# Kernel optimization log

Measured on AMD Instinct MI355X. Metric: run time of the kernel, lower is better.

Reference implementation:

```python
import jax, jax.numpy as jnp
import numpy as np

B, S, D, E = 4, 2048, 512, 32

def setup_inputs() -> dict:
    key = jax.random.key(0)
    k1, k2, k3 = jax.random.split(key, 3)
    x = jax.random.normal(k1, (B, S, D), dtype=jnp.float32)
    # glorot-ish scaling for weights
    gate_w = jax.random.normal(k2, (D, E), dtype=jnp.float32) * (1.0 / np.sqrt(D))
    gate_b = jnp.zeros((E,), dtype=jnp.float32)
    expert_w = jax.random.normal(k3, (E, D, D), dtype=jnp.float32) * (1.0 / np.sqrt(D))
    return {"x": x, "gate_w": gate_w, "gate_b": gate_b, "expert_w": expert_w}

def reference(x, gate_w, gate_b, expert_w):
    # gate_scores: [B,S,E] (context=None -> route on x itself)
    gate = jax.nn.softmax(jnp.einsum('bsd,de->bse', x, gate_w) + gate_b, axis=-1)
    # Dense soft-MoE: sum_e gate[b,s,e] * (x[b,s,:] @ expert_w[e])
    # Single einsum avoids materializing the [B,S,E,D] intermediate.
    out = jnp.einsum('bse,bsd,edf->bsf', gate, x, expert_w)
    return out
```

## Files before the change

kernel.cpp:

```cpp
#include <hip/hip_runtime.h>

#define TOK 8192
#define DIM 512
#define NE  32
#define KTOT (NE * DIM)

#define BM 128
#define BN 128
#define BK 64

typedef float f32x4 __attribute__((ext_vector_type(4)));
typedef short s16x8 __attribute__((ext_vector_type(8)));

typedef const void __attribute__((address_space(1)))* gp1_t;
typedef void __attribute__((address_space(3)))* lp3_t;

__device__ __forceinline__ void gl_lds16(const void* g, void* l) {
    __builtin_amdgcn_global_load_lds((gp1_t)g, (lp3_t)l, 16, 0, 0);
}

__device__ __forceinline__ ushort f2bf(float f) {
    unsigned u = __builtin_bit_cast(unsigned, f);
    unsigned r = (u + 0x7fffu + ((u >> 16) & 1u)) >> 16;
    return (ushort)r;
}

__global__ __launch_bounds__(256) void k_prep(const float* __restrict__ w,
                                              ushort* __restrict__ wt,
                                              const float* __restrict__ x,
                                              const float* __restrict__ gw,
                                              const float* __restrict__ gb,
                                              float* __restrict__ G,
                                              ushort* __restrict__ xb) {
    __shared__ __align__(16) char smem[64 * 65 * 4];
    const int bx = blockIdx.x;
    const int tid = threadIdx.x;
    if (bx < 2048) {
        float (*tile)[65] = (float(*)[65])smem;
        const int e = bx >> 6;
        const int f0 = ((bx >> 3) & 7) * 64;
        const int d0 = (bx & 7) * 64;
        const int tx = tid & 63, ty = tid >> 6;
        const float* we = w + (size_t)e * DIM * DIM;
#pragma unroll
        for (int i = ty; i < 64; i += 4)
            tile[i][tx] = we[(size_t)(d0 + i) * DIM + f0 + tx];
        __syncthreads();
#pragma unroll
        for (int i = ty; i < 64; i += 4)
            wt[(size_t)(f0 + i) * KTOT + e * DIM + d0 + tx] = f2bf(tile[tx][i]);
    } else {
        float* xs = (float*)smem;
        const int t0 = (bx - 2048) * 8;
        const float* xBase = x + (size_t)t0 * DIM;
#pragma unroll
        for (int k = 0; k < 4; ++k) {
            int i4 = (k * 256 + tid) * 4;
            float4 v = *(const float4*)(xBase + i4);
            xs[i4 + 0] = v.x; xs[i4 + 1] = v.y; xs[i4 + 2] = v.z; xs[i4 + 3] = v.w;
            ushort4 o;
            o.x = f2bf(v.x); o.y = f2bf(v.y); o.z = f2bf(v.z); o.w = f2bf(v.w);
            *(ushort4*)(xb + (size_t)t0 * DIM + i4) = o;
        }
        __syncthreads();
        const int tok = tid >> 5;
        const int e = tid & 31;
        float l = gb[e];
        const float* xr = xs + tok * DIM;
#pragma unroll 8
        for (int d = 0; d < DIM; ++d)
            l += xr[d] * gw[d * NE + e];
        float mx = l;
#pragma unroll
        for (int m = 16; m >= 1; m >>= 1) mx = fmaxf(mx, __shfl_xor(mx, m));
        float ex = expf(l - mx);
        float s = ex;
#pragma unroll
        for (int m = 16; m >= 1; m >>= 1) s += __shfl_xor(s, m);
        G[(size_t)(t0 + tok) * NE + e] = ex / s;
    }
}

__global__ __launch_bounds__(512, 2) void k_moe_gemm(const ushort* __restrict__ xb,
                                                     const ushort* __restrict__ wt,
                                                     const float* __restrict__ G,
                                                     float* __restrict__ out0,
                                                     float* __restrict__ out1) {
    __shared__ __align__(16) ushort As[2][BM * BK];
    __shared__ __align__(16) ushort Bs[2][BN * BK];
    __shared__ float Gs[16][BM];

    const int tid = threadIdx.x;
    const int m0 = blockIdx.y * BM;
    const int n0 = blockIdx.x * BN;
    const int e0 = blockIdx.z * 16;
    float* __restrict__ dst = blockIdx.z ? out1 : out0;

    for (int i = tid; i < 16 * BM; i += 512) {
        int e = i >> 7, r = i & 127;
        Gs[e][r] = G[(size_t)(m0 + r) * NE + e0 + e];
    }

    const int lane = tid & 63;
    const int wave = tid >> 6;
    const int wm = (wave & 3) * 32;
    const int wn = (wave >> 2) * 64;
    const int l15 = lane & 15;
    const int q = lane >> 4;
    const int keyR = l15 & 7;

    const int swz0 = ((q) ^ keyR) * 16;
    const int swz1 = ((4 + q) ^ keyR) * 16;
    const int rowA0 = (wm + l15) * 128;
    const int rowA1 = (wm + 16 + l15) * 128;
    const int rowB0 = (wn + l15) * 128;
    const int rowB1 = (wn + 16 + l15) * 128;
    const int rowB2 = (wn + 32 + l15) * 128;
    const int rowB3 = (wn + 48 + l15) * 128;

    const int srow = tid >> 3;
    const int chunk = tid & 7;
    const int scol = ((chunk ^ (srow & 7)) * 8);
    const ushort* aBase = xb + (size_t)(m0 + srow) * DIM + scol;
    const ushort* bBase = wt + (size_t)(n0 + srow) * KTOT + (size_t)e0 * DIM + scol;
    const int ldsOff = tid * 16;

    const f32x4 zv = {0.f, 0.f, 0.f, 0.f};
    f32x4 acc[2][4];
#pragma unroll
    for (int i = 0; i < 2; ++i)
#pragma unroll
        for (int j = 0; j < 4; ++j) acc[i][j] = zv;

    gl_lds16(aBase, (char*)As[0] + ldsOff);
    gl_lds16(aBase + (size_t)64 * DIM, (char*)As[0] + 8192 + ldsOff);
    gl_lds16(bBase, (char*)Bs[0] + ldsOff);
    gl_lds16(bBase + (size_t)64 * KTOT, (char*)Bs[0] + 8192 + ldsOff);
    __syncthreads();

#pragma unroll 1
    for (int kt = 0; kt < 8; ++kt) {
        const char* Ab = (const char*)As[kt & 1];
#pragma unroll 1
        for (int ee = 0; ee < 16; ++ee) {
            const int gn = kt * 16 + ee + 1;
            if (gn < 128) {
                const ushort* bN = bBase + (size_t)(gn & 15) * DIM + (gn >> 4) * BK;
                char* bL = (char*)Bs[gn & 1] + ldsOff;
                gl_lds16(bN, bL);
                gl_lds16(bN + (size_t)64 * KTOT, bL + 8192);
                if (ee == 15) {
                    const ushort* aN = aBase + (kt + 1) * BK;
                    char* aL = (char*)As[(kt + 1) & 1] + ldsOff;
                    gl_lds16(aN, aL);
                    gl_lds16(aN + (size_t)64 * DIM, aL + 8192);
                }
            }

            const char* Bb = (const char*)Bs[ee & 1];
            f32x4 pacc[2][4];
#pragma unroll
            for (int ks = 0; ks < 2; ++ks) {
                const int swz = ks ? swz1 : swz0;
                s16x8 a0 = *(const s16x8*)(Ab + rowA0 + swz);
                s16x8 a1 = *(const s16x8*)(Ab + rowA1 + swz);
                s16x8 b0 = *(const s16x8*)(Bb + rowB0 + swz);
                s16x8 b1 = *(const s16x8*)(Bb + rowB1 + swz);
                s16x8 b2 = *(const s16x8*)(Bb + rowB2 + swz);
                s16x8 b3 = *(const s16x8*)(Bb + rowB3 + swz);
                if (ks == 0) {
                    pacc[0][0] = __builtin_amdgcn_mfma_f32_16x16x32_bf16(a0, b0, zv, 0, 0, 0);
                    pacc[0][1] = __builtin_amdgcn_mfma_f32_16x16x32_bf16(a0, b1, zv, 0, 0, 0);
                    pacc[0][2] = __builtin_amdgcn_mfma_f32_16x16x32_bf16(a0, b2, zv, 0, 0, 0);
                    pacc[0][3] = __builtin_amdgcn_mfma_f32_16x16x32_bf16(a0, b3, zv, 0, 0, 0);
                    pacc[1][0] = __builtin_amdgcn_mfma_f32_16x16x32_bf16(a1, b0, zv, 0, 0, 0);
                    pacc[1][1] = __builtin_amdgcn_mfma_f32_16x16x32_bf16(a1, b1, zv, 0, 0, 0);
                    pacc[1][2] = __builtin_amdgcn_mfma_f32_16x16x32_bf16(a1, b2, zv, 0, 0, 0);
                    pacc[1][3] = __builtin_amdgcn_mfma_f32_16x16x32_bf16(a1, b3, zv, 0, 0, 0);
                } else {
                    pacc[0][0] = __builtin_amdgcn_mfma_f32_16x16x32_bf16(a0, b0, pacc[0][0], 0, 0, 0);
                    pacc[0][1] = __builtin_amdgcn_mfma_f32_16x16x32_bf16(a0, b1, pacc[0][1], 0, 0, 0);
                    pacc[0][2] = __builtin_amdgcn_mfma_f32_16x16x32_bf16(a0, b2, pacc[0][2], 0, 0, 0);
                    pacc[0][3] = __builtin_amdgcn_mfma_f32_16x16x32_bf16(a0, b3, pacc[0][3], 0, 0, 0);
                    pacc[1][0] = __builtin_amdgcn_mfma_f32_16x16x32_bf16(a1, b0, pacc[1][0], 0, 0, 0);
                    pacc[1][1] = __builtin_amdgcn_mfma_f32_16x16x32_bf16(a1, b1, pacc[1][1], 0, 0, 0);
                    pacc[1][2] = __builtin_amdgcn_mfma_f32_16x16x32_bf16(a1, b2, pacc[1][2], 0, 0, 0);
                    pacc[1][3] = __builtin_amdgcn_mfma_f32_16x16x32_bf16(a1, b3, pacc[1][3], 0, 0, 0);
                }
            }

#pragma unroll
            for (int i = 0; i < 2; ++i) {
                const f32x4 gt = *(const f32x4*)&Gs[ee][wm + i * 16 + q * 4];
#pragma unroll
                for (int j = 0; j < 4; ++j) {
                    acc[i][j][0] += gt[0] * pacc[i][j][0];
                    acc[i][j][1] += gt[1] * pacc[i][j][1];
                    acc[i][j][2] += gt[2] * pacc[i][j][2];
                    acc[i][j][3] += gt[3] * pacc[i][j][3];
                }
            }
            __syncthreads();
        }
    }

#pragma unroll
    for (int i = 0; i < 2; ++i) {
        const int tl = m0 + wm + i * 16 + q * 4;
#pragma unroll
        for (int j = 0; j < 4; ++j) {
            const int f = n0 + wn + j * 16 + l15;
            float* p = dst + (size_t)tl * DIM + f;
            p[0 * DIM] = acc[i][j][0];
            p[1 * DIM] = acc[i][j][1];
            p[2 * DIM] = acc[i][j][2];
            p[3 * DIM] = acc[i][j][3];
        }
    }
}

__global__ __launch_bounds__(256) void k_reduce(float* __restrict__ out,
                                                const float* __restrict__ P) {
    int i = (blockIdx.x * 256 + threadIdx.x) * 4;
    float4 a = *(const float4*)(out + i);
    float4 b = *(const float4*)(P + i);
    a.x += b.x; a.y += b.y; a.z += b.z; a.w += b.w;
    *(float4*)(out + i) = a;
}

extern "C" void kernel_launch(void* const* d_in, const int* in_sizes, int n_in,
                              void* d_out, int out_size, void* d_ws, size_t ws_size,
                              hipStream_t stream) {
    const float* x  = (const float*)d_in[0];
    const float* gw = (const float*)d_in[1];
    const float* gb = (const float*)d_in[2];
    const float* w  = (const float*)d_in[3];
    float* out = (float*)d_out;

    char* ws = (char*)d_ws;
    ushort* xb = (ushort*)ws;
    ushort* wt = (ushort*)(ws + (8u << 20));
    float*  G  = (float*)(ws + (24u << 20));
    float*  P  = (float*)(ws + (25u << 20));

    k_prep<<<dim3(2048 + TOK / 8), dim3(256), 0, stream>>>(w, wt, x, gw, gb, G, xb);
    k_moe_gemm<<<dim3(DIM / BN, TOK / BM, 2), dim3(512), 0, stream>>>(xb, wt, G, out, P);
    k_reduce<<<dim3(TOK * DIM / 1024), dim3(256), 0, stream>>>(out, P);
}
```

Baseline: 257.9 us.

## Switch MoE GEMM to 32x32x16 MFMA with 4 waves and register-cached A

Restructures the GEMM block from 8 waves of 32x64 tiles using 16x16x32 MFMA to 4 waves of 64x64 tiles using 32x32x16 MFMA. The A fragments are loaded from LDS once per k-tile and kept in registers across all 16 experts, and each wave reuses its operands over a larger output tile. The aim is to cut LDS reads and issue overhead per flop. In exchange, register pressure rises (4 f32x16 accumulators plus cached A) and there are fewer waves per block to hide latency.

```diff
diff --git a/kernel.cpp b/kernel.cpp
--- a/kernel.cpp
+++ b/kernel.cpp
@@ -9,14 +9,22 @@
 #define BN 128
 #define BK 64
 
-typedef float f32x4 __attribute__((ext_vector_type(4)));
-typedef short s16x8 __attribute__((ext_vector_type(8)));
+typedef float f32x4  __attribute__((ext_vector_type(4)));
+typedef float f32x16 __attribute__((ext_vector_type(16)));
+typedef short s16x8  __attribute__((ext_vector_type(8)));
 
 typedef const void __attribute__((address_space(1)))* gp1_t;
 typedef void __attribute__((address_space(3)))* lp3_t;
 
 __device__ __forceinline__ void gl_lds16(const void* g, void* l) {
     __builtin_amdgcn_global_load_lds((gp1_t)g, (lp3_t)l, 16, 0, 0);
+}
+
+__device__ __forceinline__ void stage4(const ushort* g, size_t gstride, char* l) {
+    gl_lds16(g,               l);
+    gl_lds16(g + gstride,     l + 4096);
+    gl_lds16(g + 2 * gstride, l + 8192);
+    gl_lds16(g + 3 * gstride, l + 12288);
 }
 
 __device__ __forceinline__ ushort f2bf(float f) {
@@ -81,7 +89,7 @@
     }
 }
 
-__global__ __launch_bounds__(512, 2) void k_moe_gemm(const ushort* __restrict__ xb,
+__global__ __launch_bounds__(256, 2) void k_moe_gemm(const ushort* __restrict__ xb,
                                                      const ushort* __restrict__ wt,
                                                      const float* __restrict__ G,
                                                      float* __restrict__ out0,
@@ -96,108 +104,93 @@
     const int e0 = blockIdx.z * 16;
     float* __restrict__ dst = blockIdx.z ? out1 : out0;
 
-    for (int i = tid; i < 16 * BM; i += 512) {
+    for (int i = tid; i < 16 * BM; i += 256) {
         int e = i >> 7, r = i & 127;
         Gs[e][r] = G[(size_t)(m0 + r) * NE + e0 + e];
     }
 
     const int lane = tid & 63;
     const int wave = tid >> 6;
-    const int wm = (wave & 3) * 32;
-    const int wn = (wave >> 2) * 64;
-    const int l15 = lane & 15;
-    const int q = lane >> 4;
-    const int keyR = l15 & 7;
-
-    const int swz0 = ((q) ^ keyR) * 16;
-    const int swz1 = ((4 + q) ^ keyR) * 16;
-    const int rowA0 = (wm + l15) * 128;
-    const int rowA1 = (wm + 16 + l15) * 128;
-    const int rowB0 = (wn + l15) * 128;
-    const int rowB1 = (wn + 16 + l15) * 128;
-    const int rowB2 = (wn + 32 + l15) * 128;
-    const int rowB3 = (wn + 48 + l15) * 128;
+    const int wm = (wave & 1) * 64;
+    const int wn = (wave >> 1) * 64;
+    const int l31 = lane & 31;
+    const int hi = lane >> 5;
+    const int key = l31 & 7;
+
+    int chunkOff[4], rowOffA[2], rowOffB[2];
+#pragma unroll
+    for (int s = 0; s < 4; ++s) chunkOff[s] = ((2 * s + hi) ^ key) * 16;
+#pragma unroll
+    for (int i = 0; i < 2; ++i) {
+        rowOffA[i] = (wm + i * 32 + l31) * 128;
+        rowOffB[i] = (wn + i * 32 + l31) * 128;
+    }
 
     const int srow = tid >> 3;
-    const int chunk = tid & 7;
-    const int scol = ((chunk ^ (srow & 7)) * 8);
+    const int scol = ((tid & 7) ^ (srow & 7)) * 8;
     const ushort* aBase = xb + (size_t)(m0 + srow) * DIM + scol;
     const ushort* bBase = wt + (size_t)(n0 + srow) * KTOT + (size_t)e0 * DIM + scol;
     const int ldsOff = tid * 16;
 
-    const f32x4 zv = {0.f, 0.f, 0.f, 0.f};
-    f32x4 acc[2][4];
+    f32x16 zv16;
+#pragma unroll
+    for (int j = 0; j < 16; ++j) zv16[j] = 0.f;
+    f32x16 acc[2][2];
 #pragma unroll
     for (int i = 0; i < 2; ++i)
 #pragma unroll
-        for (int j = 0; j < 4; ++j) acc[i][j] = zv;
-
-    gl_lds16(aBase, (char*)As[0] + ldsOff);
-    gl_lds16(aBase + (size_t)64 * DIM, (char*)As[0] + 8192 + ldsOff);
-    gl_lds16(bBase, (char*)Bs[0] + ldsOff);
-    gl_lds16(bBase + (size_t)64 * KTOT, (char*)Bs[0] + 8192 + ldsOff);
+        for (int j = 0; j < 2; ++j) acc[i][j] = zv16;
+
+    stage4(aBase, (size_t)32 * DIM,  (char*)As[0] + ldsOff);
+    stage4(bBase, (size_t)32 * KTOT, (char*)Bs[0] + ldsOff);
     __syncthreads();
 
 #pragma unroll 1
     for (int kt = 0; kt < 8; ++kt) {
         const char* Ab = (const char*)As[kt & 1];
+        s16x8 areg[2][4];
+#pragma unroll
+        for (int mi = 0; mi < 2; ++mi)
+#pragma unroll
+            for (int s = 0; s < 4; ++s)
+                areg[mi][s] = *(const s16x8*)(Ab + rowOffA[mi] + chunkOff[s]);
+
 #pragma unroll 1
         for (int ee = 0; ee < 16; ++ee) {
             const int gn = kt * 16 + ee + 1;
             if (gn < 128) {
                 const ushort* bN = bBase + (size_t)(gn & 15) * DIM + (gn >> 4) * BK;
-                char* bL = (char*)Bs[gn & 1] + ldsOff;
-                gl_lds16(bN, bL);
-                gl_lds16(bN + (size_t)64 * KTOT, bL + 8192);
-                if (ee == 15) {
-                    const ushort* aN = aBase + (kt + 1) * BK;
-                    char* aL = (char*)As[(kt + 1) & 1] + ldsOff;
-                    gl_lds16(aN, aL);
-                    gl_lds16(aN + (size_t)64 * DIM, aL + 8192);
+                stage4(bN, (size_t)32 * KTOT, (char*)Bs[gn & 1] + ldsOff);
+                if (ee == 15)
+                    stage4(aBase + (gn >> 4) * BK, (size_t)32 * DIM,
+                           (char*)As[(gn >> 4) & 1] + ldsOff);
+            }
+
+            const char* Bb = (const char*)Bs[ee & 1];
+            s16x8 breg[2][4];
+#pragma unroll
+            for (int nj = 0; nj < 2; ++nj)
+#pragma unroll
+                for (int s = 0; s < 4; ++s)
+                    breg[nj][s] = *(const s16x8*)(Bb + rowOffB[nj] + chunkOff[s]);
+
+#pragma unroll
+            for (int mi = 0; mi < 2; ++mi) {
+                f32x16 p0 = __builtin_amdgcn_mfma_f32_32x32x16_bf16(areg[mi][0], breg[0][0], zv16, 0, 0, 0);
+                f32x16 p1 = __builtin_amdgcn_mfma_f32_32x32x16_bf16(areg[mi][0], breg[1][0], zv16, 0, 0, 0);
+#pragma unroll
+                for (int s = 1; s < 4; ++s) {
+                    p0 = __builtin_amdgcn_mfma_f32_32x32x16_bf16(areg[mi][s], breg[0][s], p0, 0, 0, 0);
+                    p1 = __builtin_amdgcn_mfma_f32_32x32x16_bf16(areg[mi][s], breg[1][s], p1, 0, 0, 0);
                 }
-            }
-
-            const char* Bb = (const char*)Bs[ee & 1];
-            f32x4 pacc[2][4];
-#pragma unroll
-            for (int ks = 0; ks < 2; ++ks) {
-                const int swz = ks ? swz1 : swz0;
-                s16x8 a0 = *(const s16x8*)(Ab + rowA0 + swz);
-                s16x8 a1 = *(const s16x8*)(Ab + rowA1 + swz);
-                s16x8 b0 = *(const s16x8*)(Bb + rowB0 + swz);
-                s16x8 b1 = *(const s16x8*)(Bb + rowB1 + swz);
-                s16x8 b2 = *(const s16x8*)(Bb + rowB2 + swz);
-                s16x8 b3 = *(const s16x8*)(Bb + rowB3 + swz);
-                if (ks == 0) {
-                    pacc[0][0] = __builtin_amdgcn_mfma_f32_16x16x32_bf16(a0, b0, zv, 0, 0, 0);
-                    pacc[0][1] = __builtin_amdgcn_mfma_f32_16x16x32_bf16(a0, b1, zv, 0, 0, 0);
-                    pacc[0][2] = __builtin_amdgcn_mfma_f32_16x16x32_bf16(a0, b2, zv, 0, 0, 0);
-                    pacc[0][3] = __builtin_amdgcn_mfma_f32_16x16x32_bf16(a0, b3, zv, 0, 0, 0);
-                    pacc[1][0] = __builtin_amdgcn_mfma_f32_16x16x32_bf16(a1, b0, zv, 0, 0, 0);
-                    pacc[1][1] = __builtin_amdgcn_mfma_f32_16x16x32_bf16(a1, b1, zv, 0, 0, 0);
-                    pacc[1][2] = __builtin_amdgcn_mfma_f32_16x16x32_bf16(a1, b2, zv, 0, 0, 0);
-                    pacc[1][3] = __builtin_amdgcn_mfma_f32_16x16x32_bf16(a1, b3, zv, 0, 0, 0);
-                } else {
-                    pacc[0][0] = __builtin_amdgcn_mfma_f32_16x16x32_bf16(a0, b0, pacc[0][0], 0, 0, 0);
-                    pacc[0][1] = __builtin_amdgcn_mfma_f32_16x16x32_bf16(a0, b1, pacc[0][1], 0, 0, 0);
-                    pacc[0][2] = __builtin_amdgcn_mfma_f32_16x16x32_bf16(a0, b2, pacc[0][2], 0, 0, 0);
-                    pacc[0][3] = __builtin_amdgcn_mfma_f32_16x16x32_bf16(a0, b3, pacc[0][3], 0, 0, 0);
-                    pacc[1][0] = __builtin_amdgcn_mfma_f32_16x16x32_bf16(a1, b0, pacc[1][0], 0, 0, 0);
-                    pacc[1][1] = __builtin_amdgcn_mfma_f32_16x16x32_bf16(a1, b1, pacc[1][1], 0, 0, 0);
-                    pacc[1][2] = __builtin_amdgcn_mfma_f32_16x16x32_bf16(a1, b2, pacc[1][2], 0, 0, 0);
-                    pacc[1][3] = __builtin_amdgcn_mfma_f32_16x16x32_bf16(a1, b3, pacc[1][3], 0, 0, 0);
-                }
-            }
-
-#pragma unroll
-            for (int i = 0; i < 2; ++i) {
-                const f32x4 gt = *(const f32x4*)&Gs[ee][wm + i * 16 + q * 4];
-#pragma unroll
-                for (int j = 0; j < 4; ++j) {
-                    acc[i][j][0] += gt[0] * pacc[i][j][0];
-                    acc[i][j][1] += gt[1] * pacc[i][j][1];
-                    acc[i][j][2] += gt[2] * pacc[i][j][2];
-                    acc[i][j][3] += gt[3] * pacc[i][j][3];
+#pragma unroll
+                for (int g = 0; g < 4; ++g) {
+                    const f32x4 gt = *(const f32x4*)&Gs[ee][wm + mi * 32 + 8 * g + 4 * hi];
+#pragma unroll
+                    for (int j = 0; j < 4; ++j) {
+                        acc[mi][0][4 * g + j] += gt[j] * p0[4 * g + j];
+                        acc[mi][1][4 * g + j] += gt[j] * p1[4 * g + j];
+                    }
                 }
             }
             __syncthreads();
@@ -205,18 +198,19 @@
     }
 
 #pragma unroll
-    for (int i = 0; i < 2; ++i) {
-        const int tl = m0 + wm + i * 16 + q * 4;
-#pragma unroll
-        for (int j = 0; j < 4; ++j) {
-            const int f = n0 + wn + j * 16 + l15;
-            float* p = dst + (size_t)tl * DIM + f;
-            p[0 * DIM] = acc[i][j][0];
-            p[1 * DIM] = acc[i][j][1];
-            p[2 * DIM] = acc[i][j][2];
-            p[3 * DIM] = acc[i][j][3];
+    for (int mi = 0; mi < 2; ++mi)
+#pragma unroll
+        for (int nj = 0; nj < 2; ++nj) {
+            const int col = n0 + wn + nj * 32 + l31;
+#pragma unroll
+            for (int g = 0; g < 4; ++g) {
+                float* p = dst + (size_t)(m0 + wm + mi * 32 + 8 * g + 4 * hi) * DIM + col;
+                p[0 * DIM] = acc[mi][nj][4 * g + 0];
+                p[1 * DIM] = acc[mi][nj][4 * g + 1];
+                p[2 * DIM] = acc[mi][nj][4 * g + 2];
+                p[3 * DIM] = acc[mi][nj][4 * g + 3];
+            }
         }
-    }
 }
 
 __global__ __launch_bounds__(256) void k_reduce(float* __restrict__ out,
@@ -244,6 +238,6 @@
     float*  P  = (float*)(ws + (25u << 20));
 
     k_prep<<<dim3(2048 + TOK / 8), dim3(256), 0, stream>>>(w, wt, x, gw, gb, G, xb);
-    k_moe_gemm<<<dim3(DIM / BN, TOK / BM, 2), dim3(512), 0, stream>>>(xb, wt, G, out, P);
+    k_moe_gemm<<<dim3(DIM / BN, TOK / BM, 2), dim3(256), 0, stream>>>(xb, wt, G, out, P);
     k_reduce<<<dim3(TOK * DIM / 1024), dim3(256), 0, stream>>>(out, P);
 }
```

Result: no change. 259.9 us (+0.8%).
